# Kernel optimization log

Measured on AMD Instinct MI355X. Metric: run time of the kernel, lower is better.

## Reference

```python
import jax, jax.numpy as jnp
import numpy as np
from jax.scipy.linalg import solve_triangular

B, N, C = 4, 1024, 1024
H, P = 16, 5
D = C // H
CHUNK = 64
EPS = 1e-8


def l2norm(x):
    return x * jax.lax.rsqrt(jnp.sum(x * x, -1, keepdims=True) + 1e-6)


def fir_conv(x, filt):
    # x: (B,N,H,D); filt: (H,D,K); causal depthwise FIR along sequence dim
    K = filt.shape[-1]
    n = x.shape[1]
    xp = jnp.pad(x, ((0, 0), (K - 1, 0), (0, 0), (0, 0)))
    out = jnp.zeros_like(x)
    for j in range(K):  # K in {3,7}: tiny fixed tap loop
        out = out + filt[:, :, j] * xp[:, j:j + n]
    return out


def cross_mix(x, mix):
    # residual low-magnitude cross-head mixing: (H,H) matrix applied over head axis
    return x + jnp.einsum('bnhd,hg->bngd', x, mix)


def delta_rule_chunkwise(q, k, v, beta, chunk=CHUNK):
    # q,k,v: (B,H,N,D); beta: (B,H,N). Chunkwise DeltaNet recurrence.
    b, h, n, d = q.shape
    q = l2norm(q) * (d ** -0.5)
    k = l2norm(k)
    v = v * beta[..., None]
    kb = k * beta[..., None]
    nc = n // chunk
    qc, kc, vc, kbc = (t.reshape(b, h, nc, chunk, d) for t in (q, k, v, kb))
    # (I + strict-lower(kb k^T))^{-1} applied to kb and v via triangular solve
    A = jnp.tril(jnp.einsum('bhgcd,bhged->bhgce', kbc, kc), -1)
    M = A + jnp.eye(chunk, dtype=q.dtype)
    w = solve_triangular(M, kbc, lower=True)   # (B,H,nc,chunk,D)
    u = solve_triangular(M, vc, lower=True)
    attn_loc = jnp.tril(jnp.einsum('bhgcd,bhged->bhgce', qc, kc))  # causal intra-chunk

    def step(S, xs):
        q_i, k_i, w_i, u_i, a_i = xs
        u_adj = u_i - jnp.einsum('bhcd,bhde->bhce', w_i, S)
        o_i = jnp.einsum('bhcd,bhde->bhce', q_i, S) + jnp.einsum('bhce,bhed->bhcd', a_i, u_adj)
        S = S + jnp.einsum('bhcd,bhce->bhde', k_i, u_adj)
        return S, o_i

    S0 = jnp.zeros((b, h, d, d), q.dtype)
    xs = tuple(jnp.moveaxis(t, 2, 0) for t in (qc, kc, w, u, attn_loc))
    S, o = jax.lax.scan(step, S0, xs)
    o = jnp.moveaxis(o, 0, 2).reshape(b, h, n, d)
    return o, S


def setup_inputs() -> dict:
    key = jax.random.key(0)
    ks = jax.random.split(key, 12)
    s = C ** -0.5
    inp = {}
    inp['x'] = jax.random.normal(ks[0], (B, N, C), jnp.float32)
    inp['W_qkv'] = jax.random.normal(ks[1], (C, 3 * C), jnp.float32) * s
    inp['W_id'] = jax.random.normal(ks[2], (C, C), jnp.float32) * s
    inp['W_gate'] = jax.random.normal(ks[3], (C, H), jnp.float32) * s
    inp['b_gate'] = jnp.full((H,), -1.5, jnp.float32)
    inp['id_static_logit'] = jnp.full((H,), float(np.log(0.2 / 0.8)), jnp.float32)
    dirac3 = jnp.zeros((H, D, 3), jnp.float32).at[:, :, -1].set(1.0)
    dirac7 = jnp.zeros((H, D, 7), jnp.float32).at[:, :, -1].set(1.0)
    inp['fir_s'] = dirac3 + 0.02 * jax.random.normal(ks[4], (H, D, 3), jnp.float32)
    inp['fir_l'] = dirac7 + 0.02 * jax.random.normal(ks[5], (H, D, 7), jnp.float32)
    inp['mix'] = 0.02 * jax.random.normal(ks[6], (H, H), jnp.float32)
    inp['W_prune'] = jax.random.normal(ks[7], (C, H * P), jnp.float32) * s
    inp['b_prune'] = jnp.zeros((H * P,), jnp.float32)
    inp['W_g1'] = jax.random.normal(ks[8], (C, C), jnp.float32) * s
    inp['b_g1'] = jnp.zeros((C,), jnp.float32)
    inp['W_g2'] = jax.random.normal(ks[9], (C, H * P), jnp.float32) * s
    inp['b_g2'] = jnp.zeros((H * P,), jnp.float32)
    inp['W_proj'] = jax.random.normal(ks[10], (C, C), jnp.float32) * s
    inp['b_proj'] = jnp.zeros((C,), jnp.float32)
    return inp


def reference(x, W_qkv, W_id, W_gate, b_gate, id_static_logit, fir_s, fir_l, mix,
              W_prune, b_prune, W_g1, b_g1, W_g2, b_g2, W_proj, b_proj):
    b, n, c = x.shape
    qkv = (x @ W_qkv).reshape(b, n, 3, H, D).transpose(2, 0, 3, 1, 4)  # (3,B,H,N,D)
    q, k, v = qkv[0], qkv[1], qkv[2]

    # gated identity path
    identity = (x @ W_id).reshape(b, n, H, D)
    dyn_gate = jax.nn.sigmoid(x @ W_gate + b_gate)            # (B,N,H)
    id_gate = dyn_gate * jax.nn.sigmoid(id_static_logit)      # static per-head gate
    identity = identity * id_gate[..., None]

    # delta-rule branch with linearly decaying beta
    beta = jnp.broadcast_to(jnp.linspace(1.0, 0.1, n, dtype=x.dtype)[None, None, :], (b, H, n))
    delta_out, _ = delta_rule_chunkwise(q, k, v, beta)
    delta_out = delta_out.transpose(0, 2, 1, 3)               # (B,N,H,D)

    # FIR branches on V with cross-head mixing
    v_hnd = v.transpose(0, 2, 1, 3)                            # (B,N,H,D)
    fs = cross_mix(fir_conv(v_hnd, fir_s), mix)
    fl = cross_mix(fir_conv(v_hnd, fir_l), mix)

    paths = jnp.stack([fs, fl, delta_out, v_hnd, identity], axis=3)  # (B,N,H,P,D)

    # progressive pruning prior
    prune_probs = jax.nn.softmax((x @ W_prune + b_prune).reshape(b, n, H, P), -1)
    ent1 = -jnp.mean(jnp.sum(prune_probs * jnp.log(prune_probs + EPS), -1))

    # context-adaptive gating fused with pruning prior
    h = jax.nn.gelu(x @ W_g1 + b_g1)
    gate_logits = (h @ W_g2 + b_g2).reshape(b, n, H, P)
    w_gate = jax.nn.softmax(gate_logits + jnp.log(prune_probs + EPS), -1)
    ent2 = -jnp.mean(jnp.sum(w_gate * jnp.log(w_gate + EPS), -1))

    ctx = jnp.einsum('bnhp,bnhpd->bnhd', w_gate, paths)
    out = ctx.reshape(b, n, c) @ W_proj + b_proj
    return out, ent1 + ent2
```

## Files before the change

### kernel.cpp

```cpp
#include <hip/hip_runtime.h>
#include <math.h>

#define B_ 4
#define N_ 1024
#define C_ 1024
#define H_ 16
#define D_ 64
#define P_ 5
#define BN_ (B_*N_)
#define TOK 8

typedef unsigned int u32;
typedef unsigned short u16;
typedef __attribute__((ext_vector_type(8))) short bf16x8;
typedef __attribute__((ext_vector_type(4))) float f32x4;

__device__ __forceinline__ float gelu_f(float x){
  float x3 = x*x*x;
  return 0.5f*x*(1.0f + tanhf(0.7978845608028654f*(x + 0.044715f*x3)));
}
__device__ __forceinline__ float sigmoid_f(float x){ return 1.0f/(1.0f+expf(-x)); }

__device__ __forceinline__ u16 f2bf(float f) {
  u32 u = __float_as_uint(f);
  u32 r = u + 0x7fffu + ((u >> 16) & 1u);
  return (u16)(r >> 16);
}
__device__ __forceinline__ float bf2f(u16 v){ return __uint_as_float(((u32)v) << 16); }

__device__ __forceinline__ void gload16(const void* g, void* l) {
  __builtin_amdgcn_global_load_lds((const __attribute__((address_space(1))) u32*)g,
                                   (__attribute__((address_space(3))) u32*)l, 16, 0, 0);
}

__device__ __forceinline__ void trans_block(const float* __restrict__ W,
    u16* __restrict__ Wt, int K, int Nn, int roff, int bxx, int byy,
    float (*t)[33], int tid) {
  const int c0 = bxx * 32, r0 = byy * 32;
  const int tx = tid & 31, ty = tid >> 5;
  #pragma unroll
  for (int i = 0; i < 4; ++i) {
    int r = ty + i * 8;
    t[r][tx] = (c0 + tx < Nn) ? W[(size_t)(r0 + r) * Nn + c0 + tx] : 0.f;
  }
  __syncthreads();
  #pragma unroll
  for (int i = 0; i < 4; ++i) {
    int r = ty + i * 8;
    if (c0 + r < Nn)
      Wt[(size_t)(roff + c0 + r) * K + r0 + tx] = f2bf(t[tx][r]);
  }
}

__global__ __launch_bounds__(256) void setup_k(const float* __restrict__ x,
    const float* __restrict__ W_qkv, const float* __restrict__ W_id,
    const float* __restrict__ W_g1, const float* __restrict__ W_proj,
    const float* __restrict__ W_gate, const float* __restrict__ W_prune,
    const float* __restrict__ W_g2, const float* __restrict__ bg,
    const float* __restrict__ bp, const float* __restrict__ bg2,
    u16* __restrict__ xb, u16* __restrict__ wcat, u16* __restrict__ wprojT,
    u16* __restrict__ catG2, float* __restrict__ cb1, float* __restrict__ cb2,
    float* __restrict__ entA) {
  __shared__ float t[32][33];
  int bid = blockIdx.x;
  const int tid = threadIdx.x;
  if (bid < 2048) {
    int i = bid * 256 + tid;
    const float4* p = (const float4*)x + (size_t)i * 2;
    float4 a = p[0], b = p[1];
    uint4 o;
    o.x = (u32)f2bf(a.x) | ((u32)f2bf(a.y) << 16);
    o.y = (u32)f2bf(a.z) | ((u32)f2bf(a.w) << 16);
    o.z = (u32)f2bf(b.x) | ((u32)f2bf(b.y) << 16);
    o.w = (u32)f2bf(b.z) | ((u32)f2bf(b.w) << 16);
    *(uint4*)(xb + (size_t)i * 8) = o;
    return;
  }
  bid -= 2048;
  if (bid < 3072) { trans_block(W_qkv, wcat, 1024, 3072, 0, bid % 96, bid / 96, t, tid); return; }
  bid -= 3072;
  if (bid < 1024) { trans_block(W_id, wcat, 1024, 1024, 3072, bid & 31, bid >> 5, t, tid); return; }
  bid -= 1024;
  if (bid < 1024) { trans_block(W_g1, wcat, 1024, 1024, 4096, bid & 31, bid >> 5, t, tid); return; }
  bid -= 1024;
  if (bid < 1024) { trans_block(W_proj, wprojT, 1024, 1024, 0, bid & 31, bid >> 5, t, tid); return; }
  bid -= 1024;
  if (bid < 32)  { trans_block(W_gate, wcat, 1024, 16, 5120, 0, bid, t, tid); return; }
  bid -= 32;
  if (bid < 96)  { trans_block(W_prune, wcat, 1024, 80, 5136, bid % 3, bid / 3, t, tid); return; }
  bid -= 96;
  if (bid < 96)  { trans_block(W_g2, catG2, 1024, 80, 0, bid % 3, bid / 3, t, tid); return; }
  bid -= 96;
  if (bid < 8) {
    int idx = (bid * 256 + tid) * 16;
    *(uint4*)(wcat + (size_t)5216 * 1024 + idx) = make_uint4(0, 0, 0, 0);
    *(uint4*)(wcat + (size_t)5216 * 1024 + idx + 8) = make_uint4(0, 0, 0, 0);
    return;
  }
  bid -= 8;
  if (bid < 12) {
    int idx = (bid * 256 + tid) * 16;
    *(uint4*)(catG2 + 80 * 1024 + idx) = make_uint4(0, 0, 0, 0);
    *(uint4*)(catG2 + 80 * 1024 + idx + 8) = make_uint4(0, 0, 0, 0);
    return;
  }
  if (tid < 128) cb1[tid] = (tid < 16) ? bg[tid] : (tid < 96 ? bp[tid - 16] : 0.f);
  else { int c = tid - 128; cb2[c] = (c < 80) ? bg2[c] : 0.f; }
  if (tid == 0) entA[0] = 0.f;
}

template<int OBF, int NORM, int ENT>
__global__ __launch_bounds__(512, 4) void gemm_mfma2(const u16* __restrict__ A,
    const u16* __restrict__ Bt, const float* __restrict__ bias,
    float* __restrict__ Cout, int M, int Nn, int K, int Ns,
    const float* __restrict__ entSrc, float* __restrict__ entDst) {
  __shared__ __align__(16) u16 lA[3][256 * 32];
  __shared__ __align__(16) u16 lB[3][128 * 32];
  const int tid = threadIdx.x;
  const int lane = tid & 63, wid = tid >> 6;
  const int wr = wid >> 1, wc = wid & 1;
  const int r16 = lane & 15, kq = lane >> 4;
  const int row0 = blockIdx.y * 256, col0 = blockIdx.x * 128;
  const int srow = lane >> 2;
  const int skoff = (((lane & 3) ^ ((srow >> 1) & 3)) << 3);
  const int rsw = ((r16 >> 1) & 3);
  const int T = K >> 5;

  if (ENT && blockIdx.x == 0 && blockIdx.y == 0 && tid == 0)
    entDst[0] = entSrc[0] * (1.0f / 65536.0f);

  #define STAGE2(buf, tk) { \
    const int k0_ = (tk) << 5; \
    _Pragma("unroll") \
    for (int s = 0; s < 2; ++s) { \
      int c = wid * 2 + s; \
      int rt = c * 16 + srow; \
      gload16(A + (size_t)(row0 + rt) * K + k0_ + skoff, &lA[buf][c * 512]); \
    } \
    { \
      int rtB = wid * 16 + srow; \
      gload16(Bt + (size_t)(col0 + rtB) * K + k0_ + skoff, &lB[buf][wid * 512]); \
    } }

  f32x4 acc[4][4] = {};
  STAGE2(0, 0);
  STAGE2(1, 1);

  for (int t = 0; t < T; ++t) {
    if (t < T - 1) asm volatile("s_waitcnt vmcnt(3)" ::: "memory");
    else           asm volatile("s_waitcnt vmcnt(0)" ::: "memory");
    __builtin_amdgcn_s_barrier();
    asm volatile("" ::: "memory");
    if (t + 2 < T) { const int bnx = (t + 2) % 3; STAGE2(bnx, t + 2); }
    const int bc = t % 3;
    const int ko = ((kq ^ rsw) << 3);
    bf16x8 af[4], bfv[4];
    #pragma unroll
    for (int m = 0; m < 4; ++m)
      af[m] = *(const bf16x8*)&lA[bc][(wr * 64 + m * 16 + r16) * 32 + ko];
    #pragma unroll
    for (int n = 0; n < 4; ++n)
      bfv[n] = *(const bf16x8*)&lB[bc][(wc * 64 + n * 16 + r16) * 32 + ko];
    #pragma unroll
    for (int m = 0; m < 4; ++m)
      #pragma unroll
      for (int n = 0; n < 4; ++n)
        acc[m][n] = __builtin_amdgcn_mfma_f32_16x16x32_bf16(af[m], bfv[n], acc[m][n], 0, 0, 0);
  }
  #undef STAGE2

  if (NORM) {
    const int hb = (col0 + wc * 64) >> 6;
    if (hb < 32) {
      float sc[4][4];
      #pragma unroll
      for (int m = 0; m < 4; ++m)
        #pragma unroll
        for (int r = 0; r < 4; ++r) {
          float s = 0.f;
          #pragma unroll
          for (int n = 0; n < 4; ++n) s = fmaf(acc[m][n][r], acc[m][n][r], s);
          s += __shfl_xor(s, 1); s += __shfl_xor(s, 2);
          s += __shfl_xor(s, 4); s += __shfl_xor(s, 8);
          float tsc = rsqrtf(s + 1e-6f);
          sc[m][r] = (hb < 16) ? tsc * 0.125f : tsc;
        }
      #pragma unroll
      for (int m = 0; m < 4; ++m)
        #pragma unroll
        for (int n = 0; n < 4; ++n)
          #pragma unroll
          for (int r = 0; r < 4; ++r) acc[m][n][r] *= sc[m][r];
    }
  }

  #pragma unroll
  for (int n = 0; n < 4; ++n) {
    int col = col0 + wc * 64 + n * 16 + r16;
    if (col >= Ns) continue;
    float bs = bias ? bias[col] : 0.0f;
    #pragma unroll
    for (int m = 0; m < 4; ++m) {
      int rowb = row0 + wr * 64 + m * 16 + kq * 4;
      #pragma unroll
      for (int r = 0; r < 4; ++r) {
        float v = acc[m][n][r] + bs;
        if (OBF) ((u16*)Cout)[(size_t)(rowb + r) * Ns + col] = f2bf(v);
        else     Cout[(size_t)(rowb + r) * Ns + col] = v;
      }
    }
  }
}

template<int ACT, int OBF>
__global__ __launch_bounds__(256) void gemm_mfma(const u16* __restrict__ A,
    const u16* __restrict__ Bt, const float* __restrict__ bias,
    float* __restrict__ Cout, int M, int Nn, int K, int Ns) {
  __shared__ __align__(16) u16 lA[3][128 * 32];
  __shared__ __align__(16) u16 lB[3][128 * 32];
  const int tid = threadIdx.x;
  const int lane = tid & 63, wid = tid >> 6;
  const int wr = wid >> 1, wc = wid & 1;
  const int r16 = lane & 15, kq = lane >> 4;
  const int row0 = blockIdx.y * 128, col0 = blockIdx.x * 128;
  const int c0 = wid * 2;
  const int srow = lane >> 2;
  const int skoff = (((lane & 3) ^ ((srow >> 1) & 3)) << 3);
  const int rsw = ((r16 >> 1) & 3);
  const int T = K >> 5;

  #define STAGE_T(buf, tk) { \
    const int k0_ = (tk) << 5; \
    _Pragma("unroll") \
    for (int s = 0; s < 2; ++s) { \
      int c = c0 + s; \
      int rt = c * 16 + srow; \
      gload16(A  + (size_t)(row0 + rt) * K + k0_ + skoff, &lA[buf][c * 512]); \
      gload16(Bt + (size_t)(col0 + rt) * K + k0_ + skoff, &lB[buf][c * 512]); \
    } }

  f32x4 acc[4][4] = {};
  STAGE_T(0, 0);
  if (T > 1) STAGE_T(1, 1);

  for (int t = 0; t < T; ++t) {
    if (t < T - 1) asm volatile("s_waitcnt vmcnt(4)" ::: "memory");
    else           asm volatile("s_waitcnt vmcnt(0)" ::: "memory");
    __builtin_amdgcn_s_barrier();
    asm volatile("" ::: "memory");
    if (t + 2 < T) { const int bnx = (t + 2) % 3; STAGE_T(bnx, t + 2); }
    const int bc = t % 3;
    const int ko = ((kq ^ rsw) << 3);
    bf16x8 af[4], bfv[4];
    #pragma unroll
    for (int m = 0; m < 4; ++m)
      af[m] = *(const bf16x8*)&lA[bc][(wr * 64 + m * 16 + r16) * 32 + ko];
    #pragma unroll
    for (int n = 0; n < 4; ++n)
      bfv[n] = *(const bf16x8*)&lB[bc][(wc * 64 + n * 16 + r16) * 32 + ko];
    #pragma unroll
    for (int m = 0; m < 4; ++m)
      #pragma unroll
      for (int n = 0; n < 4; ++n)
        acc[m][n] = __builtin_amdgcn_mfma_f32_16x16x32_bf16(af[m], bfv[n], acc[m][n], 0, 0, 0);
  }
  #undef STAGE_T

  #pragma unroll
  for (int n = 0; n < 4; ++n) {
    int col = col0 + wc * 64 + n * 16 + r16;
    if (col >= Ns) continue;
    float bs = bias ? bias[col] : 0.0f;
    #pragma unroll
    for (int m = 0; m < 4; ++m) {
      int rowb = row0 + wr * 64 + m * 16 + kq * 4;
      #pragma unroll
      for (int r = 0; r < 4; ++r) {
        float v = acc[m][n][r] + bs;
        if (ACT == 1) v = gelu_f(v);
        if (OBF) ((u16*)Cout)[(size_t)(rowb + r) * Ns + col] = f2bf(v);
        else     Cout[(size_t)(rowb + r) * Ns + col] = v;
      }
    }
  }
}

__global__ __launch_bounds__(256) void gemm_g1gp(const u16* __restrict__ A,
    const u16* __restrict__ Bt, const float* __restrict__ b_g1,
    const float* __restrict__ cb1, u16* __restrict__ hb16,
    float* __restrict__ gp) {
  __shared__ __align__(16) u16 lA[3][128 * 32];
  __shared__ __align__(16) u16 lB[3][128 * 32];
  const int tid = threadIdx.x;
  const int lane = tid & 63, wid = tid >> 6;
  const int wr = wid >> 1, wc = wid & 1;
  const int r16 = lane & 15, kq = lane >> 4;
  const int row0 = blockIdx.y * 128, col0 = blockIdx.x * 128;
  const int K = 1024, T = 32;
  const int c0 = wid * 2;
  const int srow = lane >> 2;
  const int skoff = (((lane & 3) ^ ((srow >> 1) & 3)) << 3);
  const int rsw = ((r16 >> 1) & 3);

  #define STAGE_T(buf, tk) { \
    const int k0_ = (tk) << 5; \
    _Pragma("unroll") \
    for (int s = 0; s < 2; ++s) { \
      int c = c0 + s; \
      int rt = c * 16 + srow; \
      gload16(A  + (size_t)(row0 + rt) * K + k0_ + skoff, &lA[buf][c * 512]); \
      gload16(Bt + (size_t)(col0 + rt) * K + k0_ + skoff, &lB[buf][c * 512]); \
    } }

  f32x4 acc[4][4] = {};
  STAGE_T(0, 0);
  STAGE_T(1, 1);
  for (int t = 0; t < T; ++t) {
    if (t < T - 1) asm volatile("s_waitcnt vmcnt(4)" ::: "memory");
    else           asm volatile("s_waitcnt vmcnt(0)" ::: "memory");
    __builtin_amdgcn_s_barrier();
    asm volatile("" ::: "memory");
    if (t + 2 < T) { const int bnx = (t + 2) % 3; STAGE_T(bnx, t + 2); }
    const int bc = t % 3;
    const int ko = ((kq ^ rsw) << 3);
    bf16x8 af[4], bfv[4];
    #pragma unroll
    for (int m = 0; m < 4; ++m)
      af[m] = *(const bf16x8*)&lA[bc][(wr * 64 + m * 16 + r16) * 32 + ko];
    #pragma unroll
    for (int n = 0; n < 4; ++n)
      bfv[n] = *(const bf16x8*)&lB[bc][(wc * 64 + n * 16 + r16) * 32 + ko];
    #pragma unroll
    for (int m = 0; m < 4; ++m)
      #pragma unroll
      for (int n = 0; n < 4; ++n)
        acc[m][n] = __builtin_amdgcn_mfma_f32_16x16x32_bf16(af[m], bfv[n], acc[m][n], 0, 0, 0);
  }
  #undef STAGE_T

  const int hb = (col0 + wc * 64) >> 6;
  #pragma unroll
  for (int n = 0; n < 4; ++n) {
    const int col = col0 + wc * 64 + n * 16 + r16;
    if (hb < 16) {
      const float bs = b_g1[col];
      #pragma unroll
      for (int m = 0; m < 4; ++m) {
        int rowb = row0 + wr * 64 + m * 16 + kq * 4;
        #pragma unroll
        for (int r = 0; r < 4; ++r)
          hb16[(size_t)(rowb + r) * 1024 + col] = f2bf(gelu_f(acc[m][n][r] + bs));
      }
    } else {
      const int c2 = col - 1024;
      if (c2 < 96) {
        const float bs = cb1[c2];
        #pragma unroll
        for (int m = 0; m < 4; ++m) {
          int rowb = row0 + wr * 64 + m * 16 + kq * 4;
          #pragma unroll
          for (int r = 0; r < 4; ++r)
            gp[(size_t)(rowb + r) * 96 + c2] = acc[m][n][r] + bs;
        }
      }
    }
  }
}

__global__ __launch_bounds__(256) void delta_prep(const u16* __restrict__ qkvi,
    u16* __restrict__ tb) {
  const int bx = blockIdx.x;
  const int bh = bx >> 4, g = bx & 15;
  const int b = bh >> 4, h = bh & 15;
  const int n0 = g * 64;
  const int tid = threadIdx.x;
  __shared__ __align__(16) u16 sKb[64][72];
  __shared__ __align__(16) float sMT[64][68];
  __shared__ float sBeta[64];

  if (tid < 64) sBeta[tid] = 1.0f - 0.9f * (float)(n0 + tid) / 1023.0f;

  const int fr = tid >> 2, fe0 = (tid & 3) * 16;
  const size_t krow = ((size_t)b * N_ + n0 + fr) * 4096 + 1024 + h * 64 + fe0;
  *(uint4*)&sKb[fr][fe0]     = *(const uint4*)(qkvi + krow);
  *(uint4*)&sKb[fr][fe0 + 8] = *(const uint4*)(qkvi + krow + 8);
  __syncthreads();

  {
    const int lane = tid & 63, wv = tid >> 6;
    const int l15 = lane & 15, l4 = lane >> 4;
    bf16x8 ka0 = *(const bf16x8*)&sKb[16*wv + l15][l4*8];
    bf16x8 ka1 = *(const bf16x8*)&sKb[16*wv + l15][32 + l4*8];
    #pragma unroll
    for (int ct = 0; ct < 4; ++ct) {
      bf16x8 kc0 = *(const bf16x8*)&sKb[ct*16 + l15][l4*8];
      bf16x8 kc1 = *(const bf16x8*)&sKb[ct*16 + l15][32 + l4*8];
      f32x4 m = {};
      m = __builtin_amdgcn_mfma_f32_16x16x32_bf16(ka0, kc0, m, 0, 0, 0);
      m = __builtin_amdgcn_mfma_f32_16x16x32_bf16(ka1, kc1, m, 0, 0, 0);
      const int c = ct*16 + l15, rbase = 16*wv + l4*4;
      float4 o;
      o.x = (rbase+0 > c) ? sBeta[rbase+0] * m[0] : 0.f;
      o.y = (rbase+1 > c) ? sBeta[rbase+1] * m[1] : 0.f;
      o.z = (rbase+2 > c) ? sBeta[rbase+2] * m[2] : 0.f;
      o.w = (rbase+3 > c) ? sBeta[rbase+3] * m[3] : 0.f;
      *(float4*)&sMT[c][rbase] = o;
    }
  }
  __syncthreads();

  if (tid < 64) {
    const int c = tid;
    float a[64];
    #pragma unroll
    for (int i = 0; i < 64; ++i) a[i] = (i == c) ? 1.f : 0.f;
    #pragma unroll
    for (int ib = 0; ib < 4; ++ib) {
      #pragma unroll
      for (int i2 = 0; i2 < 16; ++i2) {
        const int i = ib * 16 + i2;
        const float wi = a[i];
        #pragma unroll
        for (int j4 = ib * 4; j4 < 16; ++j4) {
          const float4 m = *(const float4*)&sMT[i][j4 * 4];
          a[j4*4+0] = fmaf(-m.x, wi, a[j4*4+0]);
          a[j4*4+1] = fmaf(-m.y, wi, a[j4*4+1]);
          a[j4*4+2] = fmaf(-m.z, wi, a[j4*4+2]);
          a[j4*4+3] = fmaf(-m.w, wi, a[j4*4+3]);
        }
      }
    }
    const float bc = sBeta[c];
    const size_t obase = (size_t)bx * 4096;
    #pragma unroll
    for (int i = 0; i < 64; ++i) tb[obase + i * 64 + c] = f2bf(a[i] * bc);
  }
}

__global__ __launch_bounds__(256, 1) void delta_fused(const u16* __restrict__ tb,
    const u16* __restrict__ qkvi, u16* __restrict__ dOutb) {
  const int bh = blockIdx.x >> 1, h2 = blockIdx.x & 1;
  const int b = bh >> 4, h = bh & 15;
  const int dvo = h2 * 32;
  const int tid = threadIdx.x;
  const int lane = tid & 63, wv = tid >> 6;
  const int l15 = lane & 15, l4 = lane >> 4;
  const int fr = tid >> 2, fe0 = (tid & 3) * 16;
  const int fe2 = (tid & 3) * 8;

  __shared__ __align__(16) u16 sK [64][72];
  __shared__ __align__(16) u16 sKT[64][72];
  __shared__ __align__(16) u16 sT [64][72];
  __shared__ __align__(16) u16 sQ [64][72];
  __shared__ __align__(16) u16 sV [64][40];
  __shared__ __align__(16) u16 sSt[32][72];
  __shared__ __align__(16) u16 sYt[32][72];
  __shared__ __align__(16) u16 sUt[32][72];
  __shared__ __align__(16) u16 sA [64][72];

  f32x4 Sacc[2] = {};

  uint4 pk0, pk1, pt0, pt1, pq0, pq1, pv0;
  {
    const size_t bs = (size_t)(bh * 16) * 4096;
    const size_t rowq = ((size_t)(b * 1024 + fr)) * 4096 + h * 64 + fe0;
    const size_t rowv = ((size_t)(b * 1024 + fr)) * 4096 + 2048 + h * 64 + dvo + fe2;
    pq0 = *(const uint4*)(qkvi + rowq);        pq1 = *(const uint4*)(qkvi + rowq + 8);
    pk0 = *(const uint4*)(qkvi + rowq + 1024); pk1 = *(const uint4*)(qkvi + rowq + 1024 + 8);
    pv0 = *(const uint4*)(qkvi + rowv);
    pt0 = *(const uint4*)(tb + bs + tid*16);   pt1 = *(const uint4*)(tb + bs + tid*16 + 8);
  }

  for (int g = 0; g < 16; ++g) {
    __syncthreads();
    *(uint4*)&sK[fr][fe0] = pk0; *(uint4*)&sK[fr][fe0+8] = pk1;
    *(uint4*)&sT[fr][fe0] = pt0; *(uint4*)&sT[fr][fe0+8] = pt1;
    *(uint4*)&sQ[fr][fe0] = pq0; *(uint4*)&sQ[fr][fe0+8] = pq1;
    *(uint4*)&sV[fr][fe2] = pv0;
    {
      u32 kk[8] = {pk0.x, pk0.y, pk0.z, pk0.w, pk1.x, pk1.y, pk1.z, pk1.w};
      #pragma unroll
      for (int i = 0; i < 8; ++i) {
        sKT[fe0 + 2*i][fr]     = (u16)kk[i];
        sKT[fe0 + 2*i + 1][fr] = (u16)(kk[i] >> 16);
      }
    }
    #pragma unroll
    for (int dt = 0; dt < 2; ++dt) {
      u32 lo = (u32)f2bf(Sacc[dt][0]) | ((u32)f2bf(Sacc[dt][1]) << 16);
      u32 hi = (u32)f2bf(Sacc[dt][2]) | ((u32)f2bf(Sacc[dt][3]) << 16);
      *(u32*)&sSt[dt*16 + l15][16*wv + l4*4]     = lo;
      *(u32*)&sSt[dt*16 + l15][16*wv + l4*4 + 2] = hi;
    }
    __syncthreads();
    if (g < 15) {
      const size_t bs = (size_t)(bh * 16 + g + 1) * 4096;
      const size_t rowq = ((size_t)(b * 1024 + (g + 1) * 64 + fr)) * 4096 + h * 64 + fe0;
      const size_t rowv = ((size_t)(b * 1024 + (g + 1) * 64 + fr)) * 4096 + 2048 + h * 64 + dvo + fe2;
      pq0 = *(const uint4*)(qkvi + rowq);        pq1 = *(const uint4*)(qkvi + rowq + 8);
      pk0 = *(const uint4*)(qkvi + rowq + 1024); pk1 = *(const uint4*)(qkvi + rowq + 1024 + 8);
      pv0 = *(const uint4*)(qkvi + rowv);
      pt0 = *(const uint4*)(tb + bs + tid*16);   pt1 = *(const uint4*)(tb + bs + tid*16 + 8);
    }
    bf16x8 qf0 = *(const bf16x8*)&sQ[16*wv + l15][l4*8];
    bf16x8 qf1 = *(const bf16x8*)&sQ[16*wv + l15][32 + l4*8];
    bf16x8 kr0 = *(const bf16x8*)&sK[16*wv + l15][l4*8];
    bf16x8 kr1 = *(const bf16x8*)&sK[16*wv + l15][32 + l4*8];
    f32x4 aacc[4] = {}, yacc[2] = {}, oacc[2] = {};
    #pragma unroll
    for (int ct = 0; ct < 4; ++ct) {
      bf16x8 kc0 = *(const bf16x8*)&sK[ct*16 + l15][l4*8];
      bf16x8 kc1 = *(const bf16x8*)&sK[ct*16 + l15][32 + l4*8];
      aacc[ct] = __builtin_amdgcn_mfma_f32_16x16x32_bf16(qf0, kc0, aacc[ct], 0, 0, 0);
      aacc[ct] = __builtin_amdgcn_mfma_f32_16x16x32_bf16(qf1, kc1, aacc[ct], 0, 0, 0);
    }
    #pragma unroll
    for (int dt = 0; dt < 2; ++dt) {
      bf16x8 s0 = *(const bf16x8*)&sSt[dt*16 + l15][l4*8];
      bf16x8 s1 = *(const bf16x8*)&sSt[dt*16 + l15][32 + l4*8];
      yacc[dt] = __builtin_amdgcn_mfma_f32_16x16x32_bf16(kr0, s0, yacc[dt], 0, 0, 0);
      yacc[dt] = __builtin_amdgcn_mfma_f32_16x16x32_bf16(kr1, s1, yacc[dt], 0, 0, 0);
      oacc[dt] = __builtin_amdgcn_mfma_f32_16x16x32_bf16(qf0, s0, oacc[dt], 0, 0, 0);
      oacc[dt] = __builtin_amdgcn_mfma_f32_16x16x32_bf16(qf1, s1, oacc[dt], 0, 0, 0);
    }
    #pragma unroll
    for (int dt = 0; dt < 2; ++dt) {
      float y0 = bf2f(sV[16*wv + l4*4 + 0][dt*16 + l15]) - yacc[dt][0];
      float y1 = bf2f(sV[16*wv + l4*4 + 1][dt*16 + l15]) - yacc[dt][1];
      float y2 = bf2f(sV[16*wv + l4*4 + 2][dt*16 + l15]) - yacc[dt][2];
      float y3 = bf2f(sV[16*wv + l4*4 + 3][dt*16 + l15]) - yacc[dt][3];
      u32 lo = (u32)f2bf(y0) | ((u32)f2bf(y1) << 16);
      u32 hi = (u32)f2bf(y2) | ((u32)f2bf(y3) << 16);
      *(u32*)&sYt[dt*16 + l15][16*wv + l4*4]     = lo;
      *(u32*)&sYt[dt*16 + l15][16*wv + l4*4 + 2] = hi;
    }
    #pragma unroll
    for (int ct = 0; ct < 4; ++ct)
      #pragma unroll
      for (int j = 0; j < 4; ++j) {
        int r = 16*wv + l4*4 + j, c = ct*16 + l15;
        sA[r][c] = f2bf((r >= c) ? aacc[ct][j] : 0.f);
      }
    __syncthreads();
    bf16x8 tf0 = *(const bf16x8*)&sT[16*wv + l15][l4*8];
    bf16x8 tf1 = *(const bf16x8*)&sT[16*wv + l15][32 + l4*8];
    f32x4 uacc[2] = {};
    #pragma unroll
    for (int dt = 0; dt < 2; ++dt) {
      bf16x8 y0 = *(const bf16x8*)&sYt[dt*16 + l15][l4*8];
      bf16x8 y1 = *(const bf16x8*)&sYt[dt*16 + l15][32 + l4*8];
      uacc[dt] = __builtin_amdgcn_mfma_f32_16x16x32_bf16(tf0, y0, uacc[dt], 0, 0, 0);
      uacc[dt] = __builtin_amdgcn_mfma_f32_16x16x32_bf16(tf1, y1, uacc[dt], 0, 0, 0);
    }
    #pragma unroll
    for (int dt = 0; dt < 2; ++dt) {
      u32 lo = (u32)f2bf(uacc[dt][0]) | ((u32)f2bf(uacc[dt][1]) << 16);
      u32 hi = (u32)f2bf(uacc[dt][2]) | ((u32)f2bf(uacc[dt][3]) << 16);
      *(u32*)&sUt[dt*16 + l15][16*wv + l4*4]     = lo;
      *(u32*)&sUt[dt*16 + l15][16*wv + l4*4 + 2] = hi;
    }
    __syncthreads();
    bf16x8 af0 = *(const bf16x8*)&sA[16*wv + l15][l4*8];
    bf16x8 af1 = *(const bf16x8*)&sA[16*wv + l15][32 + l4*8];
    bf16x8 kt0 = *(const bf16x8*)&sKT[16*wv + l15][l4*8];
    bf16x8 kt1 = *(const bf16x8*)&sKT[16*wv + l15][32 + l4*8];
    #pragma unroll
    for (int dt = 0; dt < 2; ++dt) {
      bf16x8 u0 = *(const bf16x8*)&sUt[dt*16 + l15][l4*8];
      bf16x8 u1 = *(const bf16x8*)&sUt[dt*16 + l15][32 + l4*8];
      oacc[dt] = __builtin_amdgcn_mfma_f32_16x16x32_bf16(af0, u0, oacc[dt], 0, 0, 0);
      oacc[dt] = __builtin_amdgcn_mfma_f32_16x16x32_bf16(af1, u1, oacc[dt], 0, 0, 0);
      Sacc[dt] = __builtin_amdgcn_mfma_f32_16x16x32_bf16(kt0, u0, Sacc[dt], 0, 0, 0);
      Sacc[dt] = __builtin_amdgcn_mfma_f32_16x16x32_bf16(kt1, u1, Sacc[dt], 0, 0, 0);
    }
    #pragma unroll
    for (int dt = 0; dt < 2; ++dt)
      #pragma unroll
      for (int j = 0; j < 4; ++j) {
        int r = 16*wv + l4*4 + j;
        dOutb[((size_t)(b * 1024 + g * 64 + r)) * 1024 + h * 64 + dvo + dt*16 + l15] = f2bf(oacc[dt][j]);
      }
  }
}

__global__ __launch_bounds__(256) void paths2(const u16* __restrict__ qkvi,
    const u16* __restrict__ dOutb, const float* __restrict__ gp,
    const float* __restrict__ g2L, const float* __restrict__ fir_s,
    const float* __restrict__ fir_l, const float* __restrict__ mix,
    const float* __restrict__ idlog, u16* __restrict__ ctxb,
    float* __restrict__ entAcc) {
  const int bid = ((blockIdx.x & 7) << 6) | (blockIdx.x >> 3);
  const int b = bid >> 7, n0 = (bid & 127) * TOK;
  const int tid = threadIdx.x;
  __shared__ u16 sV[TOK + 6][1024];
  __shared__ u16 sFS[TOK][1024], sFL[TOK][1024];
  __shared__ float sMix[256];
  __shared__ float sWg[TOK][16][5];
  __shared__ float sIdg[TOK][16];
  __shared__ float sEnt[128];
  sMix[tid] = mix[tid];

  #pragma unroll
  for (int i = 0; i < 7; ++i) {
    int r = i * 2 + (tid >> 7);
    int t = n0 - 6 + r;
    int col = (tid & 127) * 8;
    uint4 v = make_uint4(0, 0, 0, 0);
    if (t >= 0)
      v = *(const uint4*)(qkvi + ((size_t)b * 1024 + t) * 4096 + 2048 + col);
    *(uint4*)&sV[r][col] = v;
  }

  if (tid < 128) {
    const int tok = tid >> 4, hh = tid & 15;
    const size_t bn = (size_t)b * 1024 + n0 + tok;
    float pl[5], lp[5];
    #pragma unroll
    for (int p = 0; p < 5; ++p) pl[p] = gp[bn * 96 + 16 + hh * 5 + p];
    float mx = pl[0];
    #pragma unroll
    for (int p = 1; p < 5; ++p) mx = fmaxf(mx, pl[p]);
    float s = 0.f;
    #pragma unroll
    for (int p = 0; p < 5; ++p) { pl[p] = expf(pl[p] - mx); s += pl[p]; }
    float inv = 1.f / s, e1 = 0.f;
    #pragma unroll
    for (int p = 0; p < 5; ++p) {
      float prob = pl[p] * inv;
      lp[p] = logf(prob + 1e-8f);
      e1 -= prob * lp[p];
    }
    float gl[5];
    #pragma unroll
    for (int p = 0; p < 5; ++p) gl[p] = g2L[bn * 80 + hh * 5 + p] + lp[p];
    float mx2 = gl[0];
    #pragma unroll
    for (int p = 1; p < 5; ++p) mx2 = fmaxf(mx2, gl[p]);
    float s2 = 0.f;
    #pragma unroll
    for (int p = 0; p < 5; ++p) { gl[p] = expf(gl[p] - mx2); s2 += gl[p]; }
    float inv2 = 1.f / s2, e2 = 0.f;
    #pragma unroll
    for (int p = 0; p < 5; ++p) {
      float w = gl[p] * inv2;
      sWg[tok][hh][p] = w;
      e2 -= w * logf(w + 1e-8f);
    }
    sEnt[tid] = e1 + e2;
    sIdg[tok][hh] = sigmoid_f(gp[bn * 96 + hh]) * sigmoid_f(idlog[hh]);
  }
  __syncthreads();

  #pragma unroll
  for (int i = 0; i < 4; ++i) {
    const int idx = tid + i * 256;
    float fl7[7], fs3[3];
    #pragma unroll
    for (int j = 0; j < 7; ++j) fl7[j] = fir_l[(size_t)idx * 7 + j];
    #pragma unroll
    for (int j = 0; j < 3; ++j) fs3[j] = fir_s[(size_t)idx * 3 + j];
    #pragma unroll
    for (int tok = 0; tok < TOK; ++tok) {
      float accs = 0.f, accl = 0.f;
      #pragma unroll
      for (int j = 0; j < 7; ++j) {
        float vv = bf2f(sV[tok + j][idx]);
        accl = fmaf(fl7[j], vv, accl);
        if (j >= 4) accs = fmaf(fs3[j - 4], vv, accs);
      }
      sFS[tok][idx] = f2bf(accs);
      sFL[tok][idx] = f2bf(accl);
    }
  }
  __syncthreads();

  #pragma unroll
  for (int i = 0; i < 4; ++i) {
    const int idx = tid + i * 256;
    const int gg = idx >> 6, d = idx & 63;
    #pragma unroll
    for (int tok = 0; tok < TOK; ++tok) {
      float as = bf2f(sFS[tok][idx]), al = bf2f(sFL[tok][idx]);
      #pragma unroll
      for (int hh = 0; hh < 16; ++hh) {
        float m = sMix[hh * 16 + gg];
        as = fmaf(bf2f(sFS[tok][hh * 64 + d]), m, as);
        al = fmaf(bf2f(sFL[tok][hh * 64 + d]), m, al);
      }
      const size_t bn = (size_t)b * 1024 + n0 + tok;
      float w0 = sWg[tok][gg][0], w1 = sWg[tok][gg][1], w2 = sWg[tok][gg][2];
      float w3 = sWg[tok][gg][3], w4 = sWg[tok][gg][4];
      float dv = bf2f(dOutb[bn * 1024 + idx]);
      float vv = bf2f(sV[tok + 6][idx]);
      float iv = bf2f(qkvi[bn * 4096 + 3072 + idx]) * sIdg[tok][gg];
      ctxb[bn * 1024 + idx] = f2bf(w0*as + w1*al + w2*dv + w3*vv + w4*iv);
    }
  }
  if (tid == 0) {
    float s = 0.f;
    #pragma unroll
    for (int i = 0; i < 128; ++i) s += sEnt[i];
    atomicAdd(entAcc, s);
  }
}

extern "C" void kernel_launch(void* const* d_in, const int* in_sizes, int n_in,
                              void* d_out, int out_size, void* d_ws, size_t ws_size,
                              hipStream_t stream) {
  (void)in_sizes; (void)n_in; (void)out_size; (void)ws_size;
  const float* x       = (const float*)d_in[0];
  const float* W_qkv   = (const float*)d_in[1];
  const float* W_id    = (const float*)d_in[2];
  const float* W_gate  = (const float*)d_in[3];
  const float* b_gate  = (const float*)d_in[4];
  const float* idlog   = (const float*)d_in[5];
  const float* fir_s   = (const float*)d_in[6];
  const float* fir_l   = (const float*)d_in[7];
  const float* mix     = (const float*)d_in[8];
  const float* W_prune = (const float*)d_in[9];
  const float* b_prune = (const float*)d_in[10];
  const float* W_g1    = (const float*)d_in[11];
  const float* b_g1    = (const float*)d_in[12];
  const float* W_g2    = (const float*)d_in[13];
  const float* b_g2    = (const float*)d_in[14];
  const float* W_proj  = (const float*)d_in[15];
  const float* b_proj  = (const float*)d_in[16];
  float* out = (float*)d_out;

  float* ws    = (float*)d_ws;
  float* qkviF = ws;
  float* gp    = ws + 8388608;
  float* g2l   = gp + 393216;
  float* kbF   = g2l + 327680;
  float* wcatF = kbF + 2097152;
  float* catG2F= wcatF + 2686976;
  float* dOb   = catG2F + 65536;
  float* entA  = dOb + 2097152;
  float* cb1   = entA + 8;
  float* cb2   = cb1 + 128;
  float* wprF  = cb2 + 128;

  u16* qkvi   = (u16*)qkviF;
  u16* wcat   = (u16*)wcatF;
  u16* tb16   = (u16*)wcatF;
  u16* catG2  = (u16*)catG2F;
  u16* dOutb  = (u16*)dOb;
  u16* wprojT = (u16*)wprF;
  u16* xb     = (u16*)kbF;
  u16* hb16   = (u16*)dOb;
  u16* ctxb   = (u16*)kbF;

  setup_k<<<8437, 256, 0, stream>>>(x, W_qkv, W_id, W_g1, W_proj, W_gate,
                                    W_prune, W_g2, b_gate, b_prune, b_g2,
                                    xb, wcat, wprojT, catG2, cb1, cb2, entA);

  gemm_mfma2<1,1,0><<<dim3(32, 16), 512, 0, stream>>>(xb, wcat, nullptr,
      (float*)qkvi, BN_, 4096, 1024, 4096, nullptr, nullptr);

  gemm_g1gp<<<dim3(9, 32), 256, 0, stream>>>(xb, wcat + (size_t)4096 * 1024,
                                             b_g1, cb1, hb16, gp);

  gemm_mfma<0,0><<<dim3(1, 32), 256, 0, stream>>>(hb16, catG2, cb2, g2l,
      BN_, 128, 1024, 80);

  delta_prep<<<1024, 256, 0, stream>>>(qkvi, tb16);
  delta_fused<<<128, 256, 0, stream>>>(tb16, qkvi, dOutb);

  paths2<<<512, 256, 0, stream>>>(qkvi, dOutb, gp, g2l,
                                  fir_s, fir_l, mix, idlog, ctxb, entA);

  gemm_mfma2<0,0,1><<<dim3(8, 16), 512, 0, stream>>>(ctxb, wprojT, b_proj, out,
      BN_, 1024, 1024, 1024, entA, out + 4194304);
}
```

Before: 233.4 us.

## Split delta recurrence across four value slices and use smaller-tile output GEMM

The delta-rule kernel now splits each (batch, head) over four 16-wide value-dimension slices instead of two, doubling the grid from 128 to 256 blocks. Each block still recomputes the full 64x64 QK^T and K-side work, but the launch fills more compute units during the sequential chunk scan. The final output projection moves from the 256x128-tile GEMM (128 blocks) to the 128x128-tile GEMM (256 blocks) to raise occupancy, so the entropy-write epilogue moves into that kernel. The cost is duplicated K/Q/T loads and A-matrix MFMAs per block.

```diff
diff --git a/kernel.cpp b/kernel.cpp
--- a/kernel.cpp
+++ b/kernel.cpp
@@ -109,11 +109,10 @@
   if (tid == 0) entA[0] = 0.f;
 }
 
-template<int OBF, int NORM, int ENT>
+template<int OBF, int NORM>
 __global__ __launch_bounds__(512, 4) void gemm_mfma2(const u16* __restrict__ A,
     const u16* __restrict__ Bt, const float* __restrict__ bias,
-    float* __restrict__ Cout, int M, int Nn, int K, int Ns,
-    const float* __restrict__ entSrc, float* __restrict__ entDst) {
+    float* __restrict__ Cout, int M, int Nn, int K, int Ns) {
   __shared__ __align__(16) u16 lA[3][256 * 32];
   __shared__ __align__(16) u16 lB[3][128 * 32];
   const int tid = threadIdx.x;
@@ -125,9 +124,6 @@
   const int skoff = (((lane & 3) ^ ((srow >> 1) & 3)) << 3);
   const int rsw = ((r16 >> 1) & 3);
   const int T = K >> 5;
-
-  if (ENT && blockIdx.x == 0 && blockIdx.y == 0 && tid == 0)
-    entDst[0] = entSrc[0] * (1.0f / 65536.0f);
 
   #define STAGE2(buf, tk) { \
     const int k0_ = (tk) << 5; \
@@ -212,10 +208,11 @@
   }
 }
 
-template<int ACT, int OBF>
+template<int ACT, int OBF, int ENT>
 __global__ __launch_bounds__(256) void gemm_mfma(const u16* __restrict__ A,
     const u16* __restrict__ Bt, const float* __restrict__ bias,
-    float* __restrict__ Cout, int M, int Nn, int K, int Ns) {
+    float* __restrict__ Cout, int M, int Nn, int K, int Ns,
+    const float* __restrict__ entSrc, float* __restrict__ entDst) {
   __shared__ __align__(16) u16 lA[3][128 * 32];
   __shared__ __align__(16) u16 lB[3][128 * 32];
   const int tid = threadIdx.x;
@@ -228,6 +225,9 @@
   const int skoff = (((lane & 3) ^ ((srow >> 1) & 3)) << 3);
   const int rsw = ((r16 >> 1) & 3);
   const int T = K >> 5;
+
+  if (ENT && blockIdx.x == 0 && blockIdx.y == 0 && tid == 0)
+    entDst[0] = entSrc[0] * (1.0f / 65536.0f);
 
   #define STAGE_T(buf, tk) { \
     const int k0_ = (tk) << 5; \
@@ -439,35 +439,36 @@
 
 __global__ __launch_bounds__(256, 1) void delta_fused(const u16* __restrict__ tb,
     const u16* __restrict__ qkvi, u16* __restrict__ dOutb) {
-  const int bh = blockIdx.x >> 1, h2 = blockIdx.x & 1;
+  const int bh = blockIdx.x >> 2, q4 = blockIdx.x & 3;
   const int b = bh >> 4, h = bh & 15;
-  const int dvo = h2 * 32;
+  const int dvo = q4 * 16;
   const int tid = threadIdx.x;
   const int lane = tid & 63, wv = tid >> 6;
   const int l15 = lane & 15, l4 = lane >> 4;
   const int fr = tid >> 2, fe0 = (tid & 3) * 16;
-  const int fe2 = (tid & 3) * 8;
+  const int fe2 = (tid & 3) * 4;
 
   __shared__ __align__(16) u16 sK [64][72];
   __shared__ __align__(16) u16 sKT[64][72];
   __shared__ __align__(16) u16 sT [64][72];
   __shared__ __align__(16) u16 sQ [64][72];
-  __shared__ __align__(16) u16 sV [64][40];
-  __shared__ __align__(16) u16 sSt[32][72];
-  __shared__ __align__(16) u16 sYt[32][72];
-  __shared__ __align__(16) u16 sUt[32][72];
+  __shared__ __align__(16) u16 sV [64][24];
+  __shared__ __align__(16) u16 sSt[16][72];
+  __shared__ __align__(16) u16 sYt[16][72];
+  __shared__ __align__(16) u16 sUt[16][72];
   __shared__ __align__(16) u16 sA [64][72];
 
-  f32x4 Sacc[2] = {};
-
-  uint4 pk0, pk1, pt0, pt1, pq0, pq1, pv0;
+  f32x4 Sacc = {};
+
+  uint4 pk0, pk1, pt0, pt1, pq0, pq1;
+  uint2 pv0;
   {
     const size_t bs = (size_t)(bh * 16) * 4096;
     const size_t rowq = ((size_t)(b * 1024 + fr)) * 4096 + h * 64 + fe0;
     const size_t rowv = ((size_t)(b * 1024 + fr)) * 4096 + 2048 + h * 64 + dvo + fe2;
     pq0 = *(const uint4*)(qkvi + rowq);        pq1 = *(const uint4*)(qkvi + rowq + 8);
     pk0 = *(const uint4*)(qkvi + rowq + 1024); pk1 = *(const uint4*)(qkvi + rowq + 1024 + 8);
-    pv0 = *(const uint4*)(qkvi + rowv);
+    pv0 = *(const uint2*)(qkvi + rowv);
     pt0 = *(const uint4*)(tb + bs + tid*16);   pt1 = *(const uint4*)(tb + bs + tid*16 + 8);
   }
 
@@ -476,7 +477,7 @@
     *(uint4*)&sK[fr][fe0] = pk0; *(uint4*)&sK[fr][fe0+8] = pk1;
     *(uint4*)&sT[fr][fe0] = pt0; *(uint4*)&sT[fr][fe0+8] = pt1;
     *(uint4*)&sQ[fr][fe0] = pq0; *(uint4*)&sQ[fr][fe0+8] = pq1;
-    *(uint4*)&sV[fr][fe2] = pv0;
+    *(uint2*)&sV[fr][fe2] = pv0;
     {
       u32 kk[8] = {pk0.x, pk0.y, pk0.z, pk0.w, pk1.x, pk1.y, pk1.z, pk1.w};
       #pragma unroll
@@ -485,12 +486,11 @@
         sKT[fe0 + 2*i + 1][fr] = (u16)(kk[i] >> 16);
       }
     }
-    #pragma unroll
-    for (int dt = 0; dt < 2; ++dt) {
-      u32 lo = (u32)f2bf(Sacc[dt][0]) | ((u32)f2bf(Sacc[dt][1]) << 16);
-      u32 hi = (u32)f2bf(Sacc[dt][2]) | ((u32)f2bf(Sacc[dt][3]) << 16);
-      *(u32*)&sSt[dt*16 + l15][16*wv + l4*4]     = lo;
-      *(u32*)&sSt[dt*16 + l15][16*wv + l4*4 + 2] = hi;
+    {
+      u32 lo = (u32)f2bf(Sacc[0]) | ((u32)f2bf(Sacc[1]) << 16);
+      u32 hi = (u32)f2bf(Sacc[2]) | ((u32)f2bf(Sacc[3]) << 16);
+      *(u32*)&sSt[l15][16*wv + l4*4]     = lo;
+      *(u32*)&sSt[l15][16*wv + l4*4 + 2] = hi;
     }
     __syncthreads();
     if (g < 15) {
@@ -499,14 +499,14 @@
       const size_t rowv = ((size_t)(b * 1024 + (g + 1) * 64 + fr)) * 4096 + 2048 + h * 64 + dvo + fe2;
       pq0 = *(const uint4*)(qkvi + rowq);        pq1 = *(const uint4*)(qkvi + rowq + 8);
       pk0 = *(const uint4*)(qkvi + rowq + 1024); pk1 = *(const uint4*)(qkvi + rowq + 1024 + 8);
-      pv0 = *(const uint4*)(qkvi + rowv);
+      pv0 = *(const uint2*)(qkvi + rowv);
       pt0 = *(const uint4*)(tb + bs + tid*16);   pt1 = *(const uint4*)(tb + bs + tid*16 + 8);
     }
     bf16x8 qf0 = *(const bf16x8*)&sQ[16*wv + l15][l4*8];
     bf16x8 qf1 = *(const bf16x8*)&sQ[16*wv + l15][32 + l4*8];
     bf16x8 kr0 = *(const bf16x8*)&sK[16*wv + l15][l4*8];
     bf16x8 kr1 = *(const bf16x8*)&sK[16*wv + l15][32 + l4*8];
-    f32x4 aacc[4] = {}, yacc[2] = {}, oacc[2] = {};
+    f32x4 aacc[4] = {}, yacc = {}, oacc = {};
     #pragma unroll
     for (int ct = 0; ct < 4; ++ct) {
       bf16x8 kc0 = *(const bf16x8*)&sK[ct*16 + l15][l4*8];
@@ -514,25 +514,23 @@
       aacc[ct] = __builtin_amdgcn_mfma_f32_16x16x32_bf16(qf0, kc0, aacc[ct], 0, 0, 0);
       aacc[ct] = __builtin_amdgcn_mfma_f32_16x16x32_bf16(qf1, kc1, aacc[ct], 0, 0, 0);
     }
-    #pragma unroll
-    for (int dt = 0; dt < 2; ++dt) {
-      bf16x8 s0 = *(const bf16x8*)&sSt[dt*16 + l15][l4*8];
-      bf16x8 s1 = *(const bf16x8*)&sSt[dt*16 + l15][32 + l4*8];
-      yacc[dt] = __builtin_amdgcn_mfma_f32_16x16x32_bf16(kr0, s0, yacc[dt], 0, 0, 0);
-      yacc[dt] = __builtin_amdgcn_mfma_f32_16x16x32_bf16(kr1, s1, yacc[dt], 0, 0, 0);
-      oacc[dt] = __builtin_amdgcn_mfma_f32_16x16x32_bf16(qf0, s0, oacc[dt], 0, 0, 0);
-      oacc[dt] = __builtin_amdgcn_mfma_f32_16x16x32_bf16(qf1, s1, oacc[dt], 0, 0, 0);
-    }
-    #pragma unroll
-    for (int dt = 0; dt < 2; ++dt) {
-      float y0 = bf2f(sV[16*wv + l4*4 + 0][dt*16 + l15]) - yacc[dt][0];
-      float y1 = bf2f(sV[16*wv + l4*4 + 1][dt*16 + l15]) - yacc[dt][1];
-      float y2 = bf2f(sV[16*wv + l4*4 + 2][dt*16 + l15]) - yacc[dt][2];
-      float y3 = bf2f(sV[16*wv + l4*4 + 3][dt*16 + l15]) - yacc[dt][3];
+    {
+      bf16x8 s0 = *(const bf16x8*)&sSt[l15][l4*8];
+      bf16x8 s1 = *(const bf16x8*)&sSt[l15][32 + l4*8];
+      yacc = __builtin_amdgcn_mfma_f32_16x16x32_bf16(kr0, s0, yacc, 0, 0, 0);
+      yacc = __builtin_amdgcn_mfma_f32_16x16x32_bf16(kr1, s1, yacc, 0, 0, 0);
+      oacc = __builtin_amdgcn_mfma_f32_16x16x32_bf16(qf0, s0, oacc, 0, 0, 0);
+      oacc = __builtin_amdgcn_mfma_f32_16x16x32_bf16(qf1, s1, oacc, 0, 0, 0);
+    }
+    {
+      float y0 = bf2f(sV[16*wv + l4*4 + 0][l15]) - yacc[0];
+      float y1 = bf2f(sV[16*wv + l4*4 + 1][l15]) - yacc[1];
+      float y2 = bf2f(sV[16*wv + l4*4 + 2][l15]) - yacc[2];
+      float y3 = bf2f(sV[16*wv + l4*4 + 3][l15]) - yacc[3];
       u32 lo = (u32)f2bf(y0) | ((u32)f2bf(y1) << 16);
       u32 hi = (u32)f2bf(y2) | ((u32)f2bf(y3) << 16);
-      *(u32*)&sYt[dt*16 + l15][16*wv + l4*4]     = lo;
-      *(u32*)&sYt[dt*16 + l15][16*wv + l4*4 + 2] = hi;
+      *(u32*)&sYt[l15][16*wv + l4*4]     = lo;
+      *(u32*)&sYt[l15][16*wv + l4*4 + 2] = hi;
     }
     #pragma unroll
     for (int ct = 0; ct < 4; ++ct)
@@ -544,42 +542,37 @@
     __syncthreads();
     bf16x8 tf0 = *(const bf16x8*)&sT[16*wv + l15][l4*8];
     bf16x8 tf1 = *(const bf16x8*)&sT[16*wv + l15][32 + l4*8];
-    f32x4 uacc[2] = {};
-    #pragma unroll
-    for (int dt = 0; dt < 2; ++dt) {
-      bf16x8 y0 = *(const bf16x8*)&sYt[dt*16 + l15][l4*8];
-      bf16x8 y1 = *(const bf16x8*)&sYt[dt*16 + l15][32 + l4*8];
-      uacc[dt] = __builtin_amdgcn_mfma_f32_16x16x32_bf16(tf0, y0, uacc[dt], 0, 0, 0);
-      uacc[dt] = __builtin_amdgcn_mfma_f32_16x16x32_bf16(tf1, y1, uacc[dt], 0, 0, 0);
-    }
-    #pragma unroll
-    for (int dt = 0; dt < 2; ++dt) {
-      u32 lo = (u32)f2bf(uacc[dt][0]) | ((u32)f2bf(uacc[dt][1]) << 16);
-      u32 hi = (u32)f2bf(uacc[dt][2]) | ((u32)f2bf(uacc[dt][3]) << 16);
-      *(u32*)&sUt[dt*16 + l15][16*wv + l4*4]     = lo;
-      *(u32*)&sUt[dt*16 + l15][16*wv + l4*4 + 2] = hi;
+    f32x4 uacc = {};
+    {
+      bf16x8 y0 = *(const bf16x8*)&sYt[l15][l4*8];
+      bf16x8 y1 = *(const bf16x8*)&sYt[l15][32 + l4*8];
+      uacc = __builtin_amdgcn_mfma_f32_16x16x32_bf16(tf0, y0, uacc, 0, 0, 0);
+      uacc = __builtin_amdgcn_mfma_f32_16x16x32_bf16(tf1, y1, uacc, 0, 0, 0);
+    }
+    {
+      u32 lo = (u32)f2bf(uacc[0]) | ((u32)f2bf(uacc[1]) << 16);
+      u32 hi = (u32)f2bf(uacc[2]) | ((u32)f2bf(uacc[3]) << 16);
+      *(u32*)&sUt[l15][16*wv + l4*4]     = lo;
+      *(u32*)&sUt[l15][16*wv + l4*4 + 2] = hi;
     }
     __syncthreads();
     bf16x8 af0 = *(const bf16x8*)&sA[16*wv + l15][l4*8];
     bf16x8 af1 = *(const bf16x8*)&sA[16*wv + l15][32 + l4*8];
     bf16x8 kt0 = *(const bf16x8*)&sKT[16*wv + l15][l4*8];
     bf16x8 kt1 = *(const bf16x8*)&sKT[16*wv + l15][32 + l4*8];
-    #pragma unroll
-    for (int dt = 0; dt < 2; ++dt) {
-      bf16x8 u0 = *(const bf16x8*)&sUt[dt*16 + l15][l4*8];
-      bf16x8 u1 = *(const bf16x8*)&sUt[dt*16 + l15][32 + l4*8];
-      oacc[dt] = __builtin_amdgcn_mfma_f32_16x16x32_bf16(af0, u0, oacc[dt], 0, 0, 0);
-      oacc[dt] = __builtin_amdgcn_mfma_f32_16x16x32_bf16(af1, u1, oacc[dt], 0, 0, 0);
-      Sacc[dt] = __builtin_amdgcn_mfma_f32_16x16x32_bf16(kt0, u0, Sacc[dt], 0, 0, 0);
-      Sacc[dt] = __builtin_amdgcn_mfma_f32_16x16x32_bf16(kt1, u1, Sacc[dt], 0, 0, 0);
-    }
-    #pragma unroll
-    for (int dt = 0; dt < 2; ++dt)
-      #pragma unroll
-      for (int j = 0; j < 4; ++j) {
-        int r = 16*wv + l4*4 + j;
-        dOutb[((size_t)(b * 1024 + g * 64 + r)) * 1024 + h * 64 + dvo + dt*16 + l15] = f2bf(oacc[dt][j]);
-      }
+    {
+      bf16x8 u0 = *(const bf16x8*)&sUt[l15][l4*8];
+      bf16x8 u1 = *(const bf16x8*)&sUt[l15][32 + l4*8];
+      oacc = __builtin_amdgcn_mfma_f32_16x16x32_bf16(af0, u0, oacc, 0, 0, 0);
+      oacc = __builtin_amdgcn_mfma_f32_16x16x32_bf16(af1, u1, oacc, 0, 0, 0);
+      Sacc = __builtin_amdgcn_mfma_f32_16x16x32_bf16(kt0, u0, Sacc, 0, 0, 0);
+      Sacc = __builtin_amdgcn_mfma_f32_16x16x32_bf16(kt1, u1, Sacc, 0, 0, 0);
+    }
+    #pragma unroll
+    for (int j = 0; j < 4; ++j) {
+      int r = 16*wv + l4*4 + j;
+      dOutb[((size_t)(b * 1024 + g * 64 + r)) * 1024 + h * 64 + dvo + l15] = f2bf(oacc[j]);
+    }
   }
 }
 
@@ -754,21 +747,21 @@
                                     W_prune, W_g2, b_gate, b_prune, b_g2,
                                     xb, wcat, wprojT, catG2, cb1, cb2, entA);
 
-  gemm_mfma2<1,1,0><<<dim3(32, 16), 512, 0, stream>>>(xb, wcat, nullptr,
-      (float*)qkvi, BN_, 4096, 1024, 4096, nullptr, nullptr);
+  gemm_mfma2<1,1><<<dim3(32, 16), 512, 0, stream>>>(xb, wcat, nullptr,
+      (float*)qkvi, BN_, 4096, 1024, 4096);
 
   gemm_g1gp<<<dim3(9, 32), 256, 0, stream>>>(xb, wcat + (size_t)4096 * 1024,
                                              b_g1, cb1, hb16, gp);
 
-  gemm_mfma<0,0><<<dim3(1, 32), 256, 0, stream>>>(hb16, catG2, cb2, g2l,
-      BN_, 128, 1024, 80);
+  gemm_mfma<0,0,0><<<dim3(1, 32), 256, 0, stream>>>(hb16, catG2, cb2, g2l,
+      BN_, 128, 1024, 80, nullptr, nullptr);
 
   delta_prep<<<1024, 256, 0, stream>>>(qkvi, tb16);
-  delta_fused<<<128, 256, 0, stream>>>(tb16, qkvi, dOutb);
+  delta_fused<<<256, 256, 0, stream>>>(tb16, qkvi, dOutb);
 
   paths2<<<512, 256, 0, stream>>>(qkvi, dOutb, gp, g2l,
                                   fir_s, fir_l, mix, idlog, ctxb, entA);
 
-  gemm_mfma2<0,0,1><<<dim3(8, 16), 512, 0, stream>>>(ctxb, wprojT, b_proj, out,
+  gemm_mfma<0,0,1><<<dim3(8, 32), 256, 0, stream>>>(ctxb, wprojT, b_proj, out,
       BN_, 1024, 1024, 1024, entA, out + 4194304);
 }
```

Result: faster. 228.3 us (-2.2%).
